# Kernel optimization log

Measured on AMD Instinct MI355X. Metric: run time of the kernel, lower is better.

The kernel has to match this reference:

```python
import jax, jax.numpy as jnp
import numpy as np

# Mamba(d_model=192) defaults from mamba_ssm
D_MODEL = 192
D_INNER = 2 * D_MODEL      # expand=2 -> 384
D_STATE = 16
D_CONV = 4
DT_RANK = (D_MODEL + 15) // 16  # 12
N_DIR = 4
LN_EPS = 1e-5


def silu(x):
    return x * jax.nn.sigmoid(x)


def mamba(x, in_proj_w, conv_w, conv_b, x_proj_w, dt_proj_w, dt_proj_b,
          A_log, D_param, out_proj_w):
    """Single-direction Mamba forward. x: [B, L, d_model]."""
    B, L, _ = x.shape
    xz = jnp.einsum('bld,ed->ble', x, in_proj_w)        # [B, L, 2*d_inner]
    u, z = jnp.split(xz, 2, axis=-1)                    # each [B, L, d_inner]
    # causal depthwise conv1d over L (groups = d_inner)
    u_c = jnp.transpose(u, (0, 2, 1))                   # [B, d_inner, L]
    kern = conv_w[:, None, :]                           # [d_inner, 1, d_conv]
    u_c = jax.lax.conv_general_dilated(
        u_c, kern, window_strides=(1,), padding=[(D_CONV - 1, 0)],
        feature_group_count=D_INNER)
    u = silu(jnp.transpose(u_c, (0, 2, 1)) + conv_b)    # [B, L, d_inner]
    # input-dependent dt, B, C
    x_dbl = jnp.einsum('ble,fe->blf', u, x_proj_w)      # [B, L, dt_rank+2*d_state]
    dt, Bc, Cc = jnp.split(x_dbl, [DT_RANK, DT_RANK + D_STATE], axis=-1)
    dt = jax.nn.softplus(jnp.einsum('blr,er->ble', dt, dt_proj_w) + dt_proj_b)
    A = -jnp.exp(A_log)                                 # [d_inner, d_state]

    def step(hst, inputs):
        dt_t, B_t, C_t, u_t = inputs  # [B,dI], [B,dS], [B,dS], [B,dI]
        dA = jnp.exp(dt_t[:, :, None] * A)              # [B, d_inner, d_state]
        hst = hst * dA + (dt_t * u_t)[:, :, None] * B_t[:, None, :]
        y_t = jnp.einsum('bes,bs->be', hst, C_t)
        return hst, y_t

    h0 = jnp.zeros((B, D_INNER, D_STATE), dtype=x.dtype)
    xs = (jnp.swapaxes(dt, 0, 1), jnp.swapaxes(Bc, 0, 1),
          jnp.swapaxes(Cc, 0, 1), jnp.swapaxes(u, 0, 1))
    _, ys = jax.lax.scan(step, h0, xs)                  # ys: [L, B, d_inner]
    y = jnp.swapaxes(ys, 0, 1) + u * D_param            # [B, L, d_inner]
    y = y * silu(z)
    return jnp.einsum('ble,de->bld', y, out_proj_w)     # [B, L, d_model]


def setup_inputs() -> dict:
    key = jax.random.key(0)
    ks = jax.random.split(key, 16)
    B, H, W = 2, 64, 64
    L = H * W
    s = 0.05
    x = jax.random.normal(ks[0], (B, L, D_MODEL), dtype=jnp.float32)
    in_proj_w = jax.random.normal(ks[1], (N_DIR, 2 * D_INNER, D_MODEL), jnp.float32) * s
    conv_w = jax.random.normal(ks[2], (N_DIR, D_INNER, D_CONV), jnp.float32) * 0.2
    conv_b = jax.random.normal(ks[3], (N_DIR, D_INNER), jnp.float32) * 0.02
    x_proj_w = jax.random.normal(ks[4], (N_DIR, DT_RANK + 2 * D_STATE, D_INNER), jnp.float32) * s
    dt_proj_w = jax.random.normal(ks[5], (N_DIR, D_INNER, DT_RANK), jnp.float32) * 0.1
    dt_proj_b = jax.random.normal(ks[6], (N_DIR, D_INNER), jnp.float32) * 0.5 - 2.0
    A_log = jnp.log(jnp.broadcast_to(
        jnp.arange(1, D_STATE + 1, dtype=jnp.float32), (N_DIR, D_INNER, D_STATE)))
    D_param = jnp.ones((N_DIR, D_INNER), jnp.float32)
    out_proj_w = jax.random.normal(ks[7], (N_DIR, D_MODEL, D_INNER), jnp.float32) * s
    ln_g = jnp.ones((D_MODEL,), jnp.float32)
    ln_b = jnp.zeros((D_MODEL,), jnp.float32)
    fuse_w = jax.random.normal(ks[8], (D_MODEL, 4 * D_MODEL), jnp.float32) * s
    fuse_b = jnp.zeros((D_MODEL,), jnp.float32)
    return {"x": x, "h": H, "w": W,
            "in_proj_w": in_proj_w, "conv_w": conv_w, "conv_b": conv_b,
            "x_proj_w": x_proj_w, "dt_proj_w": dt_proj_w, "dt_proj_b": dt_proj_b,
            "A_log": A_log, "D_param": D_param, "out_proj_w": out_proj_w,
            "ln_g": ln_g, "ln_b": ln_b, "fuse_w": fuse_w, "fuse_b": fuse_b}


def reference(x, h, w, in_proj_w, conv_w, conv_b, x_proj_w, dt_proj_w,
              dt_proj_b, A_log, D_param, out_proj_w, ln_g, ln_b, fuse_w, fuse_b):
    B, L, D = x.shape
    # LayerNorm
    mu = jnp.mean(x, axis=-1, keepdims=True)
    var = jnp.mean((x - mu) ** 2, axis=-1, keepdims=True)
    xn = (x - mu) * jax.lax.rsqrt(var + LN_EPS) * ln_g + ln_b
    # 4 directional orderings (torch.flip on [b, d, h, w] then re-flatten)
    x4 = xn.reshape(B, h, w, D)
    p1 = xn                                   # tl -> br (row-major)
    p2 = xn[:, ::-1, :]                       # flip h & w == full reverse
    p3 = x4[:, :, ::-1, :].reshape(B, L, D)   # flip w only
    p4 = x4[:, ::-1, :, :].reshape(B, L, D)   # flip h only
    ps = jnp.stack([p1, p2, p3, p4], axis=0)  # [4, B, L, D]
    outs = jax.vmap(mamba)(ps, in_proj_w, conv_w, conv_b, x_proj_w,
                           dt_proj_w, dt_proj_b, A_log, D_param, out_proj_w)
    out = jnp.concatenate([outs[0], outs[1], outs[2], outs[3]], axis=-1)  # [B,L,4D]
    out = jnp.einsum('blf,df->bld', out, fuse_w) + fuse_b
    return x + silu(out)
```

## Files before the change

kernel.cpp:

```cpp
#include <hip/hip_runtime.h>
#include <hip/hip_bf16.h>

#define L_SEQ 4096
#define DM 192
#define DI 384
#define DS 16
#define MTOT 8192
#define NC 128
#define LC 32
#define XDD 448
#define CBLK 8

typedef __attribute__((ext_vector_type(8))) short short8;
typedef __attribute__((ext_vector_type(4))) float f32x4;
typedef __hip_bfloat16 bf16;

__device__ __forceinline__ float sigm(float x){ return 1.f/(1.f+__expf(-x)); }
__device__ __forceinline__ float b2f(short s){ return __uint_as_float(((unsigned)(unsigned short)s)<<16); }

__device__ __forceinline__ void gload16(const void* g, void* l){
  __builtin_amdgcn_global_load_lds(
      (const __attribute__((address_space(1))) void*)g,
      (__attribute__((address_space(3))) void*)l, 16, 0, 0);
}

__global__ void cvt_kernel(const float* __restrict__ src, bf16* __restrict__ dst, int n){
  int i = blockIdx.x*256 + threadIdx.x;
  if (i < n) dst[i] = __float2bfloat16(src[i]);
}

__global__ void wcomb_kernel(const float* __restrict__ xpw, const float* __restrict__ dtw,
                             bf16* __restrict__ wc){
  int i = blockIdx.x*256 + threadIdx.x;
  if (i >= 4*XDD*384) return;
  int k = i % 384; int n = (i/384) % XDD; int d = i/(384*XDD);
  float v = 0.f;
  if (n < 384){
    #pragma unroll
    for (int r=0;r<12;r++) v += dtw[((size_t)d*384 + n)*12 + r] * xpw[((size_t)d*44 + r)*384 + k];
  } else if (n < 400) v = xpw[((size_t)d*44 + 12 + (n-384))*384 + k];
  else if (n < 416)   v = xpw[((size_t)d*44 + 28 + (n-400))*384 + k];
  wc[i] = __float2bfloat16(v);
}
__global__ void dtb4_kernel(const float* __restrict__ dtb, float* __restrict__ dtb4){
  int i = blockIdx.x*256 + threadIdx.x;
  if (i >= 4*XDD) return;
  int n = i % XDD, d = i / XDD;
  dtb4[i] = (n < 384) ? dtb[d*384 + n] : 0.f;
}

__global__ void ln_kernel(const float* __restrict__ x, const float* __restrict__ g,
                          const float* __restrict__ bb, bf16* __restrict__ xn){
  int row  = blockIdx.x*4 + (threadIdx.x>>6);
  int lane = threadIdx.x & 63;
  const float* xr = x + (size_t)row*DM;
  float v0 = xr[lane], v1 = xr[lane+64], v2 = xr[lane+128];
  float s = v0+v1+v2, sq = v0*v0+v1*v1+v2*v2;
  #pragma unroll
  for (int off=32; off>0; off>>=1){ s += __shfl_down(s,off); sq += __shfl_down(sq,off); }
  s = __shfl(s,0); sq = __shfl(sq,0);
  float mu  = s*(1.f/DM);
  float var = sq*(1.f/DM) - mu*mu;
  float r   = rsqrtf(var + 1e-5f);
  bf16* o = xn + (size_t)row*DM;
  o[lane]     = __float2bfloat16((v0-mu)*r*g[lane]     + bb[lane]);
  o[lane+64]  = __float2bfloat16((v1-mu)*r*g[lane+64]  + bb[lane+64]);
  o[lane+128] = __float2bfloat16((v2-mu)*r*g[lane+128] + bb[lane+128]);
}

__global__ __launch_bounds__(256) void mfma_gemm(
    const bf16* __restrict__ A, long Az,
    const bf16* __restrict__ B, long Bz,
    float* __restrict__ Cf, bf16* __restrict__ Cb, long Cz,
    int K, int ldc, int col_off, int colOffZ, int Nstore, int usePerm,
    const float* __restrict__ bias, long biasZ, const float* __restrict__ resid){
  __shared__ char lds[24576];
  char* As = lds;
  char* Bs = lds + 16384;
  int z = blockIdx.z;
  const bf16* Ap = A + (size_t)z*Az;
  const bf16* Bp = B + (size_t)z*Bz;
  int bm = blockIdx.x*128, bn = blockIdx.y*64;
  int coff = col_off + z*colOffZ;
  int perm = usePerm ? z : 0;
  int wave = threadIdx.x >> 6, lane = threadIdx.x & 63;
  int wm = wave >> 1, wn = wave & 1;
  f32x4 acc[4][2];
  #pragma unroll
  for (int m=0;m<4;m++){ acc[m][0] = (f32x4)0.f; acc[m][1] = (f32x4)0.f; }

  for (int k0 = 0; k0 < K; k0 += 64){
    #pragma unroll
    for (int j=0;j<4;j++){
      int base = (wave*4+j) << 10;
      int o = base + lane*16;
      int row = o >> 7;
      int inb = (o & 127) ^ ((row & 7) << 4);
      int m = bm + row;
      int l = m & (L_SEQ-1), mb0 = m & ~(L_SEQ-1);
      int pl;
      switch (perm){
        case 1:  pl = (L_SEQ-1) - l; break;
        case 2:  pl = (l & ~63) | (63 - (l & 63)); break;
        case 3:  pl = (4032 - (l & ~63)) | (l & 63); break;
        default: pl = l;
      }
      gload16(Ap + (size_t)(mb0+pl)*K + k0 + (inb >> 1), As + base);
    }
    #pragma unroll
    for (int j=0;j<2;j++){
      int base = (wave*2+j) << 10;
      int o = base + lane*16;
      int row = o >> 7;
      int inb = (o & 127) ^ ((row & 7) << 4);
      gload16(Bp + (size_t)(bn+row)*K + k0 + (inb >> 1), Bs + base);
    }
    __syncthreads();
    #pragma unroll
    for (int ks=0; ks<2; ++ks){
      int colb = ks*64 + ((lane>>4)<<4);
      short8 bfr[2];
      #pragma unroll
      for (int n=0;n<2;n++){
        int r = wn*32 + n*16 + (lane&15);
        bfr[n] = *(const short8*)(Bs + r*128 + (colb ^ ((r&7)<<4)));
      }
      #pragma unroll
      for (int m=0;m<4;m++){
        int r = wm*64 + m*16 + (lane&15);
        short8 af = *(const short8*)(As + r*128 + (colb ^ ((r&7)<<4)));
        acc[m][0] = __builtin_amdgcn_mfma_f32_16x16x32_bf16(af, bfr[0], acc[m][0], 0,0,0);
        acc[m][1] = __builtin_amdgcn_mfma_f32_16x16x32_bf16(af, bfr[1], acc[m][1], 0,0,0);
      }
    }
    __syncthreads();
  }
  #pragma unroll
  for (int m=0;m<4;m++){
    int row0 = bm + wm*64 + m*16 + ((lane>>4)<<2);
    #pragma unroll
    for (int n=0;n<2;n++){
      int col = wn*32 + n*16 + (lane&15);
      int gc = bn + col;
      if (gc < Nstore){
        #pragma unroll
        for (int j=0;j<4;j++){
          float v = acc[m][n][j];
          if (bias) v += bias[(size_t)z*biasZ + gc];
          size_t idx = (size_t)(row0+j)*ldc + coff + gc;
          if (resid) v = resid[idx] + v*sigm(v);
          if (Cf) Cf[(size_t)z*Cz + idx] = v;
          else    Cb[(size_t)z*Cz + idx] = __float2bfloat16(v);
        }
      }
    }
  }
}

__global__ __launch_bounds__(256) void conv_kernel(const bf16* __restrict__ xz,
    const float* __restrict__ cw, const float* __restrict__ cb, bf16* __restrict__ u){
  int dir = blockIdx.y;
  int idx = blockIdx.x*256 + threadIdx.x;
  int e8 = idx % 48;
  int t  = idx / 48;
  int lc = t & (L_SEQ/CBLK - 1), b = t / (L_SEQ/CBLK);
  int e0 = e8*8;
  int l0 = lc*CBLK;
  const bf16* src = xz + (size_t)dir*MTOT*768 + (size_t)b*L_SEQ*768 + e0;
  bf16* dst = u + (size_t)dir*MTOT*DI + ((size_t)b*L_SEQ + l0)*DI + e0;

  const float4* cw4 = (const float4*)(cw + (size_t)dir*DI*4 + e0*4);
  float w[8][4];
  #pragma unroll
  for (int q=0;q<8;q++){ float4 v = cw4[q]; w[q][0]=v.x; w[q][1]=v.y; w[q][2]=v.z; w[q][3]=v.w; }
  float bias[8];
  { const float4* cb4 = (const float4*)(cb + (size_t)dir*DI + e0);
    float4 b0 = cb4[0], b1 = cb4[1];
    bias[0]=b0.x; bias[1]=b0.y; bias[2]=b0.z; bias[3]=b0.w;
    bias[4]=b1.x; bias[5]=b1.y; bias[6]=b1.z; bias[7]=b1.w; }

  float win[3][8];
  #pragma unroll
  for (int k=0;k<3;k++){
    int l = l0 - 3 + k;
    if (l >= 0){
      short8 v = *(const short8*)(src + (size_t)l*768);
      #pragma unroll
      for (int q=0;q<8;q++) win[k][q] = b2f(v[q]);
    } else {
      #pragma unroll
      for (int q=0;q<8;q++) win[k][q] = 0.f;
    }
  }
  #pragma unroll
  for (int j=0;j<CBLK;j++){
    short8 v = *(const short8*)(src + (size_t)(l0+j)*768);
    float cur[8];
    #pragma unroll
    for (int q=0;q<8;q++) cur[q] = b2f(v[q]);
    bf16 ov[8];
    #pragma unroll
    for (int q=0;q<8;q++){
      float a = bias[q] + win[0][q]*w[q][0] + win[1][q]*w[q][1]
                        + win[2][q]*w[q][2] + cur[q]*w[q][3];
      a = a*sigm(a);
      ov[q] = __float2bfloat16(a);
    }
    *(short8*)(dst + (size_t)j*DI) = *(short8*)ov;
    #pragma unroll
    for (int q=0;q<8;q++){ win[0][q]=win[1][q]; win[1][q]=win[2][q]; win[2][q]=cur[q]; }
  }
}

template<int PASS>
__global__ __launch_bounds__(128) void scan_pass(
    const bf16* __restrict__ u_all, const bf16* __restrict__ xz_all,
    const bf16* __restrict__ xdd_all,
    const float* __restrict__ Dp,
    float* __restrict__ sumdt, float* __restrict__ hend,
    const float* __restrict__ hstart, bf16* __restrict__ y_all){
  __shared__ float smBC[LC*32];
  int bid  = blockIdx.x;
  int c    = bid % NC;
  int tmp  = bid / NC;
  int eb   = tmp % 3;
  int dirb = tmp / 3;
  int dir  = dirb >> 1, b = dirb & 1;
  int e    = eb*128 + threadIdx.x;

  const size_t S  = (size_t)MTOT*DI;
  const bf16* u   = u_all  + (size_t)dir*S;
  const bf16* xzd = xz_all + (size_t)dir*MTOT*768;
  const bf16* xdd = xdd_all + (size_t)dir*MTOT*XDD;
  bf16*       y   = y_all  + (size_t)dir*S;

  size_t mbase = (size_t)b*L_SEQ + (size_t)c*LC;

  for (int i = threadIdx.x; i < LC*32; i += 128){
    int t = i >> 5, s = i & 31;
    float v = __bfloat162float(xdd[(mbase+t)*XDD + 384 + s]);
    smBC[t*32 + ((s & 15) << 1) + (s >> 4)] = v;
  }
  __syncthreads();

  float h[DS];
  if (PASS == 1){
    #pragma unroll
    for (int s=0;s<DS;s++) h[s] = 0.f;
  } else {
    #pragma unroll
    for (int s=0;s<DS;s++)
      h[s] = hstart[(((size_t)dirb*NC + c)*DS + s)*DI + e];
  }
  float Dv = (PASS==3) ? Dp[dir*DI + e] : 0.f;
  float sdt = 0.f;

  #pragma unroll 2
  for (int t=0; t<LC; ++t){
    size_t m = mbase + t;
    float dpre = __bfloat162float(xdd[m*XDD + e]);
    float dtv = (dpre > 20.f) ? dpre : __logf(1.f + __expf(dpre));
    float uv = __bfloat162float(u[m*DI + e]);
    float du = dtv*uv;
    float r  = __expf(-dtv);
    const float2* bc = (const float2*)(smBC + t*32);
    float p = 0.f;
    float rp = r;
    #pragma unroll
    for (int s=0;s<DS;s++){
      float2 v = bc[s];
      h[s] = h[s]*rp + du*v.x;
      if (PASS==3) p += h[s]*v.y;
      rp *= r;
    }
    if (PASS==1){
      sdt += dtv;
    } else {
      float zv = __bfloat162float(xzd[m*768 + DI + e]);
      y[m*DI + e] = __float2bfloat16((p + uv*Dv) * (zv * sigm(zv)));
    }
  }

  if (PASS==1){
    sumdt[((size_t)dirb*NC + c)*DI + e] = sdt;
    #pragma unroll
    for (int s=0;s<DS;s++)
      hend[(((size_t)dirb*NC + c)*DS + s)*DI + e] = h[s];
  }
}

__global__ void carry_lo(const float* __restrict__ sumdt, const float* __restrict__ hend,
                         float* __restrict__ gH, float* __restrict__ gP){
  int i = blockIdx.x*256 + threadIdx.x;
  int e = i % DI; int q = i/DI;
  int s = q & 15; q >>= 4;
  int g = q & 7;  int dirb = q >> 3;
  float h = 0.f, gp = 1.f;
  for (int k=0;k<16;++k){
    int c = g*16 + k;
    float r = __expf(-sumdt[((size_t)dirb*NC + c)*DI + e]);
    float P = r; for (int t=0;t<s;t++) P *= r;
    h = h*P + hend[(((size_t)dirb*NC + c)*DS + s)*DI + e];
    gp *= P;
  }
  size_t o = (((size_t)dirb*8 + g)*DS + s)*DI + e;
  gH[o] = h; gP[o] = gp;
}
__global__ void carry_hi(const float* __restrict__ gH, const float* __restrict__ gP,
                         float* __restrict__ gstart){
  int i = blockIdx.x*256 + threadIdx.x;
  int e = i % DI; int q = i/DI;
  int s = q & 15; int dirb = q >> 4;
  float h = 0.f;
  for (int g=0; g<8; ++g){
    size_t o = (((size_t)dirb*8 + g)*DS + s)*DI + e;
    gstart[o] = h;
    h = h*gP[o] + gH[o];
  }
}
__global__ void carry_apply(const float* __restrict__ sumdt, const float* __restrict__ hend,
                            const float* __restrict__ gstart, float* __restrict__ hstart){
  int i = blockIdx.x*256 + threadIdx.x;
  int e = i % DI; int q = i/DI;
  int s = q & 15; q >>= 4;
  int g = q & 7;  int dirb = q >> 3;
  float h = gstart[(((size_t)dirb*8 + g)*DS + s)*DI + e];
  for (int k=0;k<16;++k){
    int c = g*16 + k;
    hstart[(((size_t)dirb*NC + c)*DS + s)*DI + e] = h;
    float r = __expf(-sumdt[((size_t)dirb*NC + c)*DI + e]);
    float P = r; for (int t=0;t<s;t++) P *= r;
    h = h*P + hend[(((size_t)dirb*NC + c)*DS + s)*DI + e];
  }
}

extern "C" void kernel_launch(void* const* d_in, const int* in_sizes, int n_in,
                              void* d_out, int out_size, void* d_ws, size_t ws_size,
                              hipStream_t stream){
  const float* x    = (const float*)d_in[0];
  const float* ipw  = (const float*)d_in[3];
  const float* cw   = (const float*)d_in[4];
  const float* cb   = (const float*)d_in[5];
  const float* xpw  = (const float*)d_in[6];
  const float* dtw  = (const float*)d_in[7];
  const float* dtb  = (const float*)d_in[8];
  const float* Dp   = (const float*)d_in[10];
  const float* opw  = (const float*)d_in[11];
  const float* lng  = (const float*)d_in[12];
  const float* lnb  = (const float*)d_in[13];
  const float* fw   = (const float*)d_in[14];
  const float* fb   = (const float*)d_in[15];
  float* out = (float*)d_out;

  char* p = (char*)d_ws;
  auto alloc = [&](size_t bytes)->char*{ char* r = p; p += (bytes + 255) & ~255UL; return r; };
  bf16*  xn    = (bf16*) alloc((size_t)MTOT*DM*2);
  bf16*  xz    = (bf16*) alloc(4UL*MTOT*768*2);
  bf16*  u     = (bf16*) alloc(4UL*MTOT*DI*2);
  bf16*  xdd   = (bf16*) alloc(4UL*MTOT*XDD*2);
  bf16*  ycat  = (bf16*) alloc((size_t)MTOT*768*2);
  bf16*  ipwb  = (bf16*) alloc(4UL*768*192*2);
  bf16*  opwb  = (bf16*) alloc(4UL*192*384*2);
  bf16*  wcomb = (bf16*) alloc(4UL*XDD*384*2);
  bf16*  fwb   = (bf16*) alloc(192UL*768*2);
  float* dtb4  = (float*)alloc(4UL*XDD*4);
  float* sumdt = (float*)alloc(8UL*NC*DI*4);
  float* hend  = (float*)alloc(8UL*NC*DS*DI*4);
  float* hstart= (float*)alloc(8UL*NC*DS*DI*4);
  float* gH    = (float*)alloc(8UL*8*DS*DI*4);
  float* gP    = (float*)alloc(8UL*8*DS*DI*4);
  float* gstart= (float*)alloc(8UL*8*DS*DI*4);

  dim3 blk(256);
  cvt_kernel<<<(4*768*192+255)/256, blk, 0, stream>>>(ipw, ipwb, 4*768*192);
  cvt_kernel<<<(4*192*384+255)/256, blk, 0, stream>>>(opw, opwb, 4*192*384);
  cvt_kernel<<<(192*768+255)/256,   blk, 0, stream>>>(fw,  fwb,  192*768);
  wcomb_kernel<<<(4*XDD*384+255)/256, blk, 0, stream>>>(xpw, dtw, wcomb);
  dtb4_kernel<<<(4*XDD+255)/256, blk, 0, stream>>>(dtb, dtb4);

  ln_kernel<<<MTOT/4, blk, 0, stream>>>(x, lng, lnb, xn);

  mfma_gemm<<<dim3(64,12,4), blk, 0, stream>>>(xn, 0L, ipwb, 768L*192,
      nullptr, xz, (long)MTOT*768, 192, 768, 0, 0, 768, 1, nullptr, 0L, nullptr);

  conv_kernel<<<dim3((4*MTOT*48/CBLK/8)/256 ? (MTOT/CBLK*48)/256 : 1, 4), blk, 0, stream>>>(xz, cw, cb, u);

  mfma_gemm<<<dim3(64,7,4), blk, 0, stream>>>(u, (long)MTOT*DI, wcomb, (long)XDD*384,
      nullptr, xdd, (long)MTOT*XDD, 384, XDD, 0, 0, XDD, 0, dtb4, (long)XDD, nullptr);

  scan_pass<1><<<8*3*NC, dim3(128), 0, stream>>>(u, xz, xdd, Dp,
                                                 sumdt, hend, nullptr, nullptr);
  carry_lo<<<(8*8*DS*DI)/256, blk, 0, stream>>>(sumdt, hend, gH, gP);
  carry_hi<<<(8*DS*DI)/256, blk, 0, stream>>>(gH, gP, gstart);
  carry_apply<<<(8*8*DS*DI)/256, blk, 0, stream>>>(sumdt, hend, gstart, hstart);
  scan_pass<3><<<8*3*NC, dim3(128), 0, stream>>>(u, xz, xdd, Dp,
                                                 nullptr, nullptr, hstart, u);

  mfma_gemm<<<dim3(64,3,4), blk, 0, stream>>>(u, (long)MTOT*DI, opwb, 192L*384,
      nullptr, ycat, 0L, 384, 768, 0, 192, 192, 0, nullptr, 0L, nullptr);

  mfma_gemm<<<dim3(64,3,1), blk, 0, stream>>>(ycat, 0L, fwb, 0L,
      out, nullptr, 0L, 768, 192, 0, 0, 192, 0, fb, 0L, x);
}
```

Before: 250.2 us.

## Cache decay and dt*u from scan pass 1 as half2, vectorize state update

Pass 1 of the chunked scan now stores exp(-dt) and dt*u for each element as an fp16 half2 buffer, so pass 3 reads them back instead of recomputing softplus and exp. The state update is rewritten on float2 vectors, computing two decay powers at once so packed FMA can be used, and the B/C shared-memory layout becomes contiguous. The conv grid expression is also simplified. This adds a 32 MB write and read of extra global traffic. It also lowers the precision of the decay and input terms to fp16, which risks accuracy loss, for example underflow of small dt*u.

```diff
diff --git a/kernel.cpp b/kernel.cpp
--- a/kernel.cpp
+++ b/kernel.cpp
@@ -1,5 +1,6 @@
 #include <hip/hip_runtime.h>
 #include <hip/hip_bf16.h>
+#include <hip/hip_fp16.h>
 
 #define L_SEQ 4096
 #define DM 192
@@ -13,6 +14,7 @@
 
 typedef __attribute__((ext_vector_type(8))) short short8;
 typedef __attribute__((ext_vector_type(4))) float f32x4;
+typedef __attribute__((ext_vector_type(2))) float f32x2;
 typedef __hip_bfloat16 bf16;
 
 __device__ __forceinline__ float sigm(float x){ return 1.f/(1.f+__expf(-x)); }
@@ -215,7 +217,7 @@
 template<int PASS>
 __global__ __launch_bounds__(128) void scan_pass(
     const bf16* __restrict__ u_all, const bf16* __restrict__ xz_all,
-    const bf16* __restrict__ xdd_all,
+    const bf16* __restrict__ xdd_all, __half2* __restrict__ rdu_all,
     const float* __restrict__ Dp,
     float* __restrict__ sumdt, float* __restrict__ hend,
     const float* __restrict__ hstart, bf16* __restrict__ y_all){
@@ -232,25 +234,25 @@
   const bf16* u   = u_all  + (size_t)dir*S;
   const bf16* xzd = xz_all + (size_t)dir*MTOT*768;
   const bf16* xdd = xdd_all + (size_t)dir*MTOT*XDD;
+  __half2*   rdu  = rdu_all + (size_t)dir*S;
   bf16*       y   = y_all  + (size_t)dir*S;
 
   size_t mbase = (size_t)b*L_SEQ + (size_t)c*LC;
 
-  for (int i = threadIdx.x; i < LC*32; i += 128){
-    int t = i >> 5, s = i & 31;
-    float v = __bfloat162float(xdd[(mbase+t)*XDD + 384 + s]);
-    smBC[t*32 + ((s & 15) << 1) + (s >> 4)] = v;
-  }
+  for (int i = threadIdx.x; i < LC*32; i += 128)
+    smBC[i] = __bfloat162float(xdd[(mbase + (i>>5))*XDD + 384 + (i&31)]);
   __syncthreads();
 
-  float h[DS];
+  f32x2 h2[8];
   if (PASS == 1){
     #pragma unroll
-    for (int s=0;s<DS;s++) h[s] = 0.f;
+    for (int k=0;k<8;k++) h2[k] = (f32x2)0.f;
   } else {
     #pragma unroll
-    for (int s=0;s<DS;s++)
-      h[s] = hstart[(((size_t)dirb*NC + c)*DS + s)*DI + e];
+    for (int k=0;k<8;k++){
+      h2[k][0] = hstart[(((size_t)dirb*NC + c)*DS + 2*k  )*DI + e];
+      h2[k][1] = hstart[(((size_t)dirb*NC + c)*DS + 2*k+1)*DI + e];
+    }
   }
   float Dv = (PASS==3) ? Dp[dir*DI + e] : 0.f;
   float sdt = 0.f;
@@ -258,34 +260,48 @@
   #pragma unroll 2
   for (int t=0; t<LC; ++t){
     size_t m = mbase + t;
-    float dpre = __bfloat162float(xdd[m*XDD + e]);
-    float dtv = (dpre > 20.f) ? dpre : __logf(1.f + __expf(dpre));
-    float uv = __bfloat162float(u[m*DI + e]);
-    float du = dtv*uv;
-    float r  = __expf(-dtv);
-    const float2* bc = (const float2*)(smBC + t*32);
-    float p = 0.f;
-    float rp = r;
-    #pragma unroll
-    for (int s=0;s<DS;s++){
-      float2 v = bc[s];
-      h[s] = h[s]*rp + du*v.x;
-      if (PASS==3) p += h[s]*v.y;
-      rp *= r;
-    }
-    if (PASS==1){
+    float r, du, uv;
+    if (PASS == 1){
+      float dpre = __bfloat162float(xdd[m*XDD + e]);
+      float dtv = (dpre > 20.f) ? dpre : __logf(1.f + __expf(dpre));
+      uv = __bfloat162float(u[m*DI + e]);
+      du = dtv*uv;
+      r  = __expf(-dtv);
+      rdu[m*DI + e] = __halves2half2(__float2half(r), __float2half(du));
       sdt += dtv;
     } else {
+      __half2 rd = rdu[m*DI + e];
+      r  = __low2float(rd);
+      du = __high2float(rd);
+      uv = __bfloat162float(u[m*DI + e]);
+    }
+    float rr = r*r;
+    f32x2 rp2; rp2[0] = r; rp2[1] = rr;
+    f32x2 r2;  r2[0] = rr; r2[1] = rr;
+    f32x2 du2; du2[0] = du; du2[1] = du;
+    const f32x2* b2 = (const f32x2*)(smBC + t*32);
+    const f32x2* c2 = (const f32x2*)(smBC + t*32 + 16);
+    f32x2 p2 = (f32x2)0.f;
+    #pragma unroll
+    for (int k=0;k<8;k++){
+      h2[k] = h2[k]*rp2 + du2*b2[k];
+      if (PASS==3) p2 += h2[k]*c2[k];
+      rp2 *= r2;
+    }
+    if (PASS==3){
+      float pp = p2[0] + p2[1];
       float zv = __bfloat162float(xzd[m*768 + DI + e]);
-      y[m*DI + e] = __float2bfloat16((p + uv*Dv) * (zv * sigm(zv)));
+      y[m*DI + e] = __float2bfloat16((pp + uv*Dv) * (zv * sigm(zv)));
     }
   }
 
   if (PASS==1){
     sumdt[((size_t)dirb*NC + c)*DI + e] = sdt;
     #pragma unroll
-    for (int s=0;s<DS;s++)
-      hend[(((size_t)dirb*NC + c)*DS + s)*DI + e] = h[s];
+    for (int k=0;k<8;k++){
+      hend[(((size_t)dirb*NC + c)*DS + 2*k  )*DI + e] = h2[k][0];
+      hend[(((size_t)dirb*NC + c)*DS + 2*k+1)*DI + e] = h2[k][1];
+    }
   }
 }
 
@@ -358,6 +374,7 @@
   bf16*  xz    = (bf16*) alloc(4UL*MTOT*768*2);
   bf16*  u     = (bf16*) alloc(4UL*MTOT*DI*2);
   bf16*  xdd   = (bf16*) alloc(4UL*MTOT*XDD*2);
+  __half2* rdu = (__half2*)alloc(4UL*MTOT*DI*4);
   bf16*  ycat  = (bf16*) alloc((size_t)MTOT*768*2);
   bf16*  ipwb  = (bf16*) alloc(4UL*768*192*2);
   bf16*  opwb  = (bf16*) alloc(4UL*192*384*2);
@@ -383,17 +400,17 @@
   mfma_gemm<<<dim3(64,12,4), blk, 0, stream>>>(xn, 0L, ipwb, 768L*192,
       nullptr, xz, (long)MTOT*768, 192, 768, 0, 0, 768, 1, nullptr, 0L, nullptr);
 
-  conv_kernel<<<dim3((4*MTOT*48/CBLK/8)/256 ? (MTOT/CBLK*48)/256 : 1, 4), blk, 0, stream>>>(xz, cw, cb, u);
+  conv_kernel<<<dim3((MTOT/CBLK*48)/256, 4), blk, 0, stream>>>(xz, cw, cb, u);
 
   mfma_gemm<<<dim3(64,7,4), blk, 0, stream>>>(u, (long)MTOT*DI, wcomb, (long)XDD*384,
       nullptr, xdd, (long)MTOT*XDD, 384, XDD, 0, 0, XDD, 0, dtb4, (long)XDD, nullptr);
 
-  scan_pass<1><<<8*3*NC, dim3(128), 0, stream>>>(u, xz, xdd, Dp,
+  scan_pass<1><<<8*3*NC, dim3(128), 0, stream>>>(u, xz, xdd, rdu, Dp,
                                                  sumdt, hend, nullptr, nullptr);
   carry_lo<<<(8*8*DS*DI)/256, blk, 0, stream>>>(sumdt, hend, gH, gP);
   carry_hi<<<(8*DS*DI)/256, blk, 0, stream>>>(gH, gP, gstart);
   carry_apply<<<(8*8*DS*DI)/256, blk, 0, stream>>>(sumdt, hend, gstart, hstart);
-  scan_pass<3><<<8*3*NC, dim3(128), 0, stream>>>(u, xz, xdd, Dp,
+  scan_pass<3><<<8*3*NC, dim3(128), 0, stream>>>(u, xz, xdd, rdu, Dp,
                                                  nullptr, nullptr, hstart, u);
 
   mfma_gemm<<<dim3(64,3,4), blk, 0, stream>>>(u, (long)MTOT*DI, opwb, 192L*384,
```

New measurement: 235.1 us. 6.0% less time.

## Process two channels per thread in scan passes and merge weight conversions

Applied to the files above, without the earlier changes.

The chunked selective-scan passes are restructured so each 192-thread block covers all 384 inner channels, with every thread handling two adjacent channels through vectorized loads and stores. The B/C staging in shared memory is now loaded once per block instead of once per 128-channel slice. Pass 1 stages only B. The state-decay powers are split into even and odd chains to shorten the dependency chain. The three weight-conversion launches are merged into one, cutting launch overhead, at the cost of a third as many scan blocks, which lowers parallelism, and higher register pressure.

```diff
diff --git a/kernel.cpp b/kernel.cpp
--- a/kernel.cpp
+++ b/kernel.cpp
@@ -13,6 +13,7 @@
 
 typedef __attribute__((ext_vector_type(8))) short short8;
 typedef __attribute__((ext_vector_type(4))) float f32x4;
+typedef __attribute__((ext_vector_type(2))) float f32x2;
 typedef __hip_bfloat16 bf16;
 
 __device__ __forceinline__ float sigm(float x){ return 1.f/(1.f+__expf(-x)); }
@@ -24,9 +25,15 @@
       (__attribute__((address_space(3))) void*)l, 16, 0, 0);
 }
 
-__global__ void cvt_kernel(const float* __restrict__ src, bf16* __restrict__ dst, int n){
-  int i = blockIdx.x*256 + threadIdx.x;
-  if (i < n) dst[i] = __float2bfloat16(src[i]);
+__global__ void cvt3_kernel(const float* __restrict__ s1, bf16* __restrict__ d1, int n1,
+                            const float* __restrict__ s2, bf16* __restrict__ d2, int n2,
+                            const float* __restrict__ s3, bf16* __restrict__ d3, int n3){
+  int i = blockIdx.x*256 + threadIdx.x;
+  if (i < n1){ d1[i] = __float2bfloat16(s1[i]); return; }
+  i -= n1;
+  if (i < n2){ d2[i] = __float2bfloat16(s2[i]); return; }
+  i -= n2;
+  if (i < n3) d3[i] = __float2bfloat16(s3[i]);
 }
 
 __global__ void wcomb_kernel(const float* __restrict__ xpw, const float* __restrict__ dtw,
@@ -213,20 +220,20 @@
 }
 
 template<int PASS>
-__global__ __launch_bounds__(128) void scan_pass(
+__global__ __launch_bounds__(192) void scan_pass(
     const bf16* __restrict__ u_all, const bf16* __restrict__ xz_all,
     const bf16* __restrict__ xdd_all,
     const float* __restrict__ Dp,
     float* __restrict__ sumdt, float* __restrict__ hend,
     const float* __restrict__ hstart, bf16* __restrict__ y_all){
+  const int BCW = (PASS==1) ? 16 : 32;
   __shared__ float smBC[LC*32];
   int bid  = blockIdx.x;
-  int c    = bid % NC;
-  int tmp  = bid / NC;
-  int eb   = tmp % 3;
-  int dirb = tmp / 3;
+  int c    = bid & (NC-1);
+  int dirb = bid >> 7;
   int dir  = dirb >> 1, b = dirb & 1;
-  int e    = eb*128 + threadIdx.x;
+  int tid  = threadIdx.x;
+  int e0   = tid*2;
 
   const size_t S  = (size_t)MTOT*DI;
   const bf16* u   = u_all  + (size_t)dir*S;
@@ -236,56 +243,81 @@
 
   size_t mbase = (size_t)b*L_SEQ + (size_t)c*LC;
 
-  for (int i = threadIdx.x; i < LC*32; i += 128){
-    int t = i >> 5, s = i & 31;
-    float v = __bfloat162float(xdd[(mbase+t)*XDD + 384 + s]);
-    smBC[t*32 + ((s & 15) << 1) + (s >> 4)] = v;
+  for (int i = tid; i < LC*(BCW/2); i += 192){
+    int t = i/(BCW/2), j = (i - t*(BCW/2))*2;
+    short2 v = *(const short2*)(xdd + (mbase+t)*XDD + 384 + j);
+    smBC[t*BCW + j]   = b2f(v.x);
+    smBC[t*BCW + j+1] = b2f(v.y);
   }
   __syncthreads();
 
-  float h[DS];
+  size_t hbase = (((size_t)dirb*NC + c)*DS)*DI + e0;
+  f32x2 h[DS];
   if (PASS == 1){
     #pragma unroll
-    for (int s=0;s<DS;s++) h[s] = 0.f;
+    for (int s=0;s<DS;s++) h[s] = (f32x2)0.f;
   } else {
     #pragma unroll
-    for (int s=0;s<DS;s++)
-      h[s] = hstart[(((size_t)dirb*NC + c)*DS + s)*DI + e];
-  }
-  float Dv = (PASS==3) ? Dp[dir*DI + e] : 0.f;
-  float sdt = 0.f;
-
-  #pragma unroll 2
+    for (int s=0;s<DS;s++) h[s] = *(const f32x2*)(hstart + hbase + (size_t)s*DI);
+  }
+  f32x2 Dv = (PASS==3) ? *(const f32x2*)(Dp + dir*DI + e0) : (f32x2)0.f;
+  f32x2 sdt = (f32x2)0.f;
+
   for (int t=0; t<LC; ++t){
     size_t m = mbase + t;
-    float dpre = __bfloat162float(xdd[m*XDD + e]);
-    float dtv = (dpre > 20.f) ? dpre : __logf(1.f + __expf(dpre));
-    float uv = __bfloat162float(u[m*DI + e]);
-    float du = dtv*uv;
-    float r  = __expf(-dtv);
-    const float2* bc = (const float2*)(smBC + t*32);
-    float p = 0.f;
-    float rp = r;
-    #pragma unroll
-    for (int s=0;s<DS;s++){
-      float2 v = bc[s];
-      h[s] = h[s]*rp + du*v.x;
-      if (PASS==3) p += h[s]*v.y;
-      rp *= r;
-    }
+    short2 d2 = *(const short2*)(xdd + m*XDD + e0);
+    short2 u2 = *(const short2*)(u + m*DI + e0);
+    float dp0 = b2f(d2.x), dp1 = b2f(d2.y);
+    float dt0 = (dp0 > 20.f) ? dp0 : __logf(1.f + __expf(dp0));
+    float dt1 = (dp1 > 20.f) ? dp1 : __logf(1.f + __expf(dp1));
+    f32x2 uv; uv[0] = b2f(u2.x); uv[1] = b2f(u2.y);
+    f32x2 dt2; dt2[0] = dt0; dt2[1] = dt1;
+    f32x2 du2 = dt2*uv;
+    f32x2 rv; rv[0] = __expf(-dt0); rv[1] = __expf(-dt1);
+    f32x2 rsq = rv*rv;
+
+    float Bs[DS], Cs[DS];
+    { const f32x4* p4 = (const f32x4*)(smBC + t*BCW);
+      #pragma unroll
+      for (int j=0;j<4;j++){ f32x4 v4 = p4[j];
+        Bs[4*j]=v4[0]; Bs[4*j+1]=v4[1]; Bs[4*j+2]=v4[2]; Bs[4*j+3]=v4[3]; }
+      if (PASS==3){
+        #pragma unroll
+        for (int j=0;j<4;j++){ f32x4 v4 = p4[4+j];
+          Cs[4*j]=v4[0]; Cs[4*j+1]=v4[1]; Cs[4*j+2]=v4[2]; Cs[4*j+3]=v4[3]; }
+      }
+    }
+
+    f32x2 rpE = rv, rpO = rsq;
+    f32x2 pE = (f32x2)0.f, pO = (f32x2)0.f;
+    #pragma unroll
+    for (int k=0;k<8;k++){
+      int sE = 2*k, sO = 2*k+1;
+      h[sE] = h[sE]*rpE + du2*Bs[sE];
+      h[sO] = h[sO]*rpO + du2*Bs[sO];
+      if (PASS==3){ pE += h[sE]*Cs[sE]; pO += h[sO]*Cs[sO]; }
+      rpE *= rsq; rpO *= rsq;
+    }
+
     if (PASS==1){
-      sdt += dtv;
+      sdt += dt2;
     } else {
-      float zv = __bfloat162float(xzd[m*768 + DI + e]);
-      y[m*DI + e] = __float2bfloat16((p + uv*Dv) * (zv * sigm(zv)));
+      short2 z2 = *(const short2*)(xzd + m*768 + DI + e0);
+      f32x2 pp = pE + pO;
+      float y0, y1;
+      { float zv = b2f(z2.x); y0 = (pp[0] + uv[0]*Dv[0]) * (zv*sigm(zv)); }
+      { float zv = b2f(z2.y); y1 = (pp[1] + uv[1]*Dv[1]) * (zv*sigm(zv)); }
+      union { short2 s2; bf16 bb[2]; } o;
+      o.bb[0] = __float2bfloat16(y0); o.bb[1] = __float2bfloat16(y1);
+      *(short2*)(y + m*DI + e0) = o.s2;
     }
   }
 
   if (PASS==1){
-    sumdt[((size_t)dirb*NC + c)*DI + e] = sdt;
+    *(f32x2*)(sumdt + ((size_t)dirb*NC + c)*DI + e0) = sdt;
     #pragma unroll
     for (int s=0;s<DS;s++)
-      hend[(((size_t)dirb*NC + c)*DS + s)*DI + e] = h[s];
+      *(f32x2*)(hend + hbase + (size_t)s*DI) = h[s];
   }
 }
 
@@ -372,9 +404,8 @@
   float* gstart= (float*)alloc(8UL*8*DS*DI*4);
 
   dim3 blk(256);
-  cvt_kernel<<<(4*768*192+255)/256, blk, 0, stream>>>(ipw, ipwb, 4*768*192);
-  cvt_kernel<<<(4*192*384+255)/256, blk, 0, stream>>>(opw, opwb, 4*192*384);
-  cvt_kernel<<<(192*768+255)/256,   blk, 0, stream>>>(fw,  fwb,  192*768);
+  const int n1 = 4*768*192, n2 = 4*192*384, n3 = 192*768;
+  cvt3_kernel<<<(n1+n2+n3+255)/256, blk, 0, stream>>>(ipw, ipwb, n1, opw, opwb, n2, fw, fwb, n3);
   wcomb_kernel<<<(4*XDD*384+255)/256, blk, 0, stream>>>(xpw, dtw, wcomb);
   dtb4_kernel<<<(4*XDD+255)/256, blk, 0, stream>>>(dtb, dtb4);
 
@@ -383,18 +414,18 @@
   mfma_gemm<<<dim3(64,12,4), blk, 0, stream>>>(xn, 0L, ipwb, 768L*192,
       nullptr, xz, (long)MTOT*768, 192, 768, 0, 0, 768, 1, nullptr, 0L, nullptr);
 
-  conv_kernel<<<dim3((4*MTOT*48/CBLK/8)/256 ? (MTOT/CBLK*48)/256 : 1, 4), blk, 0, stream>>>(xz, cw, cb, u);
+  conv_kernel<<<dim3((MTOT/CBLK*48)/256, 4), blk, 0, stream>>>(xz, cw, cb, u);
 
   mfma_gemm<<<dim3(64,7,4), blk, 0, stream>>>(u, (long)MTOT*DI, wcomb, (long)XDD*384,
       nullptr, xdd, (long)MTOT*XDD, 384, XDD, 0, 0, XDD, 0, dtb4, (long)XDD, nullptr);
 
-  scan_pass<1><<<8*3*NC, dim3(128), 0, stream>>>(u, xz, xdd, Dp,
-                                                 sumdt, hend, nullptr, nullptr);
+  scan_pass<1><<<8*NC, dim3(192), 0, stream>>>(u, xz, xdd, Dp,
+                                               sumdt, hend, nullptr, nullptr);
   carry_lo<<<(8*8*DS*DI)/256, blk, 0, stream>>>(sumdt, hend, gH, gP);
   carry_hi<<<(8*DS*DI)/256, blk, 0, stream>>>(gH, gP, gstart);
   carry_apply<<<(8*8*DS*DI)/256, blk, 0, stream>>>(sumdt, hend, gstart, hstart);
-  scan_pass<3><<<8*3*NC, dim3(128), 0, stream>>>(u, xz, xdd, Dp,
-                                                 nullptr, nullptr, hstart, u);
+  scan_pass<3><<<8*NC, dim3(192), 0, stream>>>(u, xz, xdd, Dp,
+                                               nullptr, nullptr, hstart, u);
 
   mfma_gemm<<<dim3(64,3,4), blk, 0, stream>>>(u, (long)MTOT*DI, opwb, 192L*384,
       nullptr, ycat, 0L, 384, 768, 0, 192, 192, 0, nullptr, 0L, nullptr);
```

Measured after the change: 243.1 us. 1.03x faster.
